# Kernel tuning notes

Measured on AMD Instinct MI355X. Metric: run time of the kernel, lower is better.

Reference implementation:

```python
import jax, jax.numpy as jnp
import numpy as np

FR = 44100          # frame_rate
L = 882000          # sound length (20 s @ 44.1 kHz)
T = 2048            # number of onset time steps
H_GRU = 3
H_LSTM = 10


def setup_inputs() -> dict:
    key = jax.random.key(0)
    ks = jax.random.split(key, 20)

    def unif(k, shape, fan):
        b = 1.0 / np.sqrt(fan)
        return jax.random.uniform(k, shape, jnp.float32, -b, b)

    return {
        "sound": jax.random.normal(ks[0], (1, L), jnp.float32),
        "alpha": jnp.sort(jax.random.randint(ks[1], (1, T), 0, L), axis=1),
        # GRU (input_size=FR, hidden=3): gates ordered (r, z, n). W_hh is
        # multiplied by h0=0 (seq_len==1), so only its bias b_hh matters.
        "gru_w_ih": unif(ks[2], (3 * H_GRU, FR), H_GRU),
        "gru_b_ih": unif(ks[3], (3 * H_GRU,), H_GRU),
        "gru_b_hh": unif(ks[4], (3 * H_GRU,), H_GRU),
        "conv2_w": unif(ks[5], (32, 1, 3), 1 * 3),
        "conv2_b": unif(ks[6], (32,), 1 * 3),
        "conv3_w": unif(ks[7], (16, 32, 3), 32 * 3),
        "conv3_b": unif(ks[8], (16,), 32 * 3),
        "lin_w": unif(ks[9], (10, 17), 17),
        "lin_b": unif(ks[10], (10,), 17),
        # LSTMCell gates ordered (i, f, g, o)
        "lstm_w_ih": unif(ks[11], (4 * H_LSTM, 10), H_LSTM),
        "lstm_w_hh": unif(ks[12], (4 * H_LSTM, H_LSTM), H_LSTM),
        "lstm_b_ih": unif(ks[13], (4 * H_LSTM,), H_LSTM),
        "lstm_b_hh": unif(ks[14], (4 * H_LSTM,), H_LSTM),
        "lin1_w": unif(ks[15], (32, 10), 10),
        "lin1_b": unif(ks[16], (32,), 10),
        "lin2_w": unif(ks[17], (1, 32), 32),
        "lin2_b": unif(ks[18], (1,), 32),
    }


def _conv1d(x, w, b, pad):
    # x: (N, C_in, W), w: (C_out, C_in, K)
    y = jax.lax.conv_general_dilated(
        x, w, window_strides=(1,), padding=[(pad, pad)],
        dimension_numbers=("NCH", "OIH", "NCH"))
    return y + b[None, :, None]


def reference(sound, alpha, gru_w_ih, gru_b_ih, gru_b_hh,
              conv2_w, conv2_b, conv3_w, conv3_b, lin_w, lin_b,
              lstm_w_ih, lstm_w_hh, lstm_b_ih, lstm_b_hh,
              lin1_w, lin1_b, lin2_w, lin2_b):
    fr2 = FR // 2
    padded = jnp.pad(sound[0], (fr2, fr2))                       # (L + FR,)
    # Vectorized dynamic-window gather: one (T, FR) fragment matrix.
    idx = alpha[0][:, None] + jnp.arange(FR)[None, :]            # (T, FR)
    frags = jnp.abs(padded[idx])                                 # (T, FR)

    # GRU: batch=1 -> unbatched input of seq_len=1, h0=0 => single step.
    gi = frags @ gru_w_ih.T + gru_b_ih                           # (T, 9)
    r = jax.nn.sigmoid(gi[:, 0:3] + gru_b_hh[0:3])
    z = jax.nn.sigmoid(gi[:, 3:6] + gru_b_hh[3:6])
    n = jnp.tanh(gi[:, 6:9] + r * gru_b_hh[6:9])
    h = (1.0 - z) * n                                            # (T, 3)

    x = h[:, None, :]                                            # (T, 1, 3)
    x = jax.nn.relu(_conv1d(x, conv2_w, conv2_b, pad=1))         # (T, 32, 3)
    x = _conv1d(x, conv3_w, conv3_b, pad=0)                      # (T, 16, 1)
    feat = x[:, :, 0]                                            # (T, 16)

    a = alpha[0].astype(jnp.float32)
    intervals = jnp.concatenate([a[:1], a[1:] - a[:-1]])         # (T,)
    xin = jnp.concatenate([intervals[:, None], feat], axis=1)    # (T, 17)
    xin = xin @ lin_w.T + lin_b                                  # (T, 10)

    def step(carry, xt):
        hh, cc = carry
        g = xt @ lstm_w_ih.T + lstm_b_ih + hh @ lstm_w_hh.T + lstm_b_hh
        i, f, gg, o = jnp.split(g, 4)
        cc = jax.nn.sigmoid(f) * cc + jax.nn.sigmoid(i) * jnp.tanh(gg)
        hh = jax.nn.sigmoid(o) * jnp.tanh(cc)
        return (hh, cc), None

    init = (jnp.zeros(H_LSTM, jnp.float32), jnp.zeros(H_LSTM, jnp.float32))
    (hT, _), _ = jax.lax.scan(step, init, xin)                   # hT: (10,)

    y = jax.nn.relu(hT[None, :] @ lin1_w.T + lin1_b)             # (1, 32)
    return jax.nn.sigmoid(y @ lin2_w.T + lin2_b)                 # (1, 1)
```

## Files before the change

kernel.cpp:

```cpp
#include <hip/hip_runtime.h>

#define FRLEN 44100
#define FR2 22050
#define LSND 882000
#define PADLEN (LSND + FRLEN)
#define TSTEPS 2048
#define ROWS 8
#define LOG2E 1.4426950408889634f

#define KPAD 44104
#define WPROW (KPAD/2)
#define NJP (WPROW/4)
#define PAIRS 463056

typedef _Float16 half2_ __attribute__((ext_vector_type(2)));

__device__ __forceinline__ float sigmoidf_(float x){ return 1.0f/(1.0f + __expf(-x)); }

__device__ __forceinline__ float dot2u_(uint a, uint b, float c){
#if __has_builtin(__builtin_amdgcn_fdot2)
  return __builtin_amdgcn_fdot2(*(half2_*)&a, *(half2_*)&b, c, false);
#else
  half2_ ha = *(half2_*)&a, hb = *(half2_*)&b;
  c = fmaf((float)ha.x, (float)hb.x, c);
  return fmaf((float)ha.y, (float)hb.y, c);
#endif
}

__device__ __forceinline__ float dot2h_(half2_ a, half2_ b, float c){
#if __has_builtin(__builtin_amdgcn_fdot2)
  return __builtin_amdgcn_fdot2(a, b, c, false);
#else
  c = fmaf((float)a.x, (float)b.x, c);
  return fmaf((float)a.y, (float)b.y, c);
#endif
}

__global__ void k_prep16(const float* __restrict__ sound, const float* __restrict__ w,
                         uint* __restrict__ pA, uint* __restrict__ pB,
                         uint* __restrict__ wp){
  const int stride = gridDim.x*blockDim.x;
  for (int i = blockIdx.x*blockDim.x + threadIdx.x; i < PAIRS + 9*WPROW; i += stride){
    if (i < PAIRS){
      int e0 = 2*i - FR2;
      float v0 = (e0 >= 0     && e0 < LSND)     ? fabsf(sound[e0])   : 0.0f;
      float v1 = (e0+1 >= 0   && e0+1 < LSND)   ? fabsf(sound[e0+1]) : 0.0f;
      float v2 = (e0+2 >= 0   && e0+2 < LSND)   ? fabsf(sound[e0+2]) : 0.0f;
      half2_ a = { (_Float16)v0, (_Float16)v1 };
      half2_ b = { (_Float16)v1, (_Float16)v2 };
      pA[i] = *(uint*)&a;
      pB[i] = *(uint*)&b;
    } else {
      int p = i - PAIRS;
      int k = p / WPROW, pr = p % WPROW;
      int j = 2*pr;
      float v0 = (j   < FRLEN) ? w[k*FRLEN + j]   : 0.0f;
      float v1 = (j+1 < FRLEN) ? w[k*FRLEN + j+1] : 0.0f;
      half2_ a = { (_Float16)v0, (_Float16)v1 };
      wp[i - PAIRS] = *(uint*)&a;
    }
  }
}

__global__ __launch_bounds__(512, 2) void k_front(const uint* __restrict__ pA,
    const uint* __restrict__ pB, const uint* __restrict__ wp,
    const int* __restrict__ alpha,
    const float* __restrict__ gbih, const float* __restrict__ gbhh,
    const float* __restrict__ c2w, const float* __restrict__ c2b,
    const float* __restrict__ c3w, const float* __restrict__ c3b,
    const float* __restrict__ lw, const float* __restrict__ lb,
    const float* __restrict__ wih, const float* __restrict__ bih, const float* __restrict__ bhh,
    _Float16* __restrict__ pre){
  const int tid = threadIdx.x;
  const int row0 = blockIdx.x * ROWS;
  const uint* hp[ROWS];
  int idx0[ROWS];
#pragma unroll
  for (int r = 0; r < ROWS; ++r){
    int b = alpha[row0 + r];
    hp[r] = (b & 1) ? pB : pA;
    idx0[r] = b >> 1;
  }
  float acc[ROWS][9];
#pragma unroll
  for (int r = 0; r < ROWS; ++r)
#pragma unroll
    for (int k = 0; k < 9; ++k) acc[r][k] = 0.0f;

  for (int jj = tid; jj < NJP; jj += 512){
    const int jp = jj*4;
    uint4 f[ROWS];
#pragma unroll
    for (int r = 0; r < ROWS; ++r){
      const uint* p = hp[r] + idx0[r] + jp;
      f[r].x = p[0]; f[r].y = p[1]; f[r].z = p[2]; f[r].w = p[3];
    }
#pragma unroll
    for (int k = 0; k < 9; ++k){
      const uint4 wq = *reinterpret_cast<const uint4*>(wp + k*WPROW + jp);
#pragma unroll
      for (int r = 0; r < ROWS; ++r){
        acc[r][k] = dot2u_(f[r].x, wq.x, acc[r][k]);
        acc[r][k] = dot2u_(f[r].y, wq.y, acc[r][k]);
        acc[r][k] = dot2u_(f[r].z, wq.z, acc[r][k]);
        acc[r][k] = dot2u_(f[r].w, wq.w, acc[r][k]);
      }
    }
  }
#pragma unroll
  for (int m = 32; m >= 1; m >>= 1){
#pragma unroll
    for (int r = 0; r < ROWS; ++r)
#pragma unroll
      for (int k = 0; k < 9; ++k)
        acc[r][k] += __shfl_xor(acc[r][k], m, 64);
  }
  __shared__ float red[8][ROWS*9];
  __shared__ float sgi[ROWS*9];
  const int wv_ = tid >> 6, ln = tid & 63;
  if (ln == 0){
#pragma unroll
    for (int r = 0; r < ROWS; ++r)
#pragma unroll
      for (int k = 0; k < 9; ++k) red[wv_][r*9+k] = acc[r][k];
  }
  __syncthreads();
  if (tid < ROWS*9){
    float s = 0.0f;
#pragma unroll
    for (int q = 0; q < 8; ++q) s += red[q][tid];
    sgi[tid] = s;
  }
  __syncthreads();
  if (tid < ROWS){
    const int t = row0 + tid;
    float gi[9];
#pragma unroll
    for (int k = 0; k < 9; ++k) gi[k] = sgi[tid*9+k] + gbih[k];
    float h[3];
#pragma unroll
    for (int q = 0; q < 3; ++q){
      float rr = sigmoidf_(gi[q]   + gbhh[q]);
      float zz = sigmoidf_(gi[3+q] + gbhh[3+q]);
      float nn = tanhf(gi[6+q] + rr*gbhh[6+q]);
      h[q] = (1.0f - zz)*nn;
    }
    float feat[16];
#pragma unroll
    for (int c = 0; c < 16; ++c) feat[c] = c3b[c];
    for (int ic = 0; ic < 32; ++ic){
      float w0 = c2w[ic*3+0], w1 = c2w[ic*3+1], w2 = c2w[ic*3+2], bb = c2b[ic];
      float x0 = fmaxf(bb + h[0]*w1 + h[1]*w2, 0.0f);
      float x1 = fmaxf(bb + h[0]*w0 + h[1]*w1 + h[2]*w2, 0.0f);
      float x2_ = fmaxf(bb + h[1]*w0 + h[2]*w1, 0.0f);
#pragma unroll
      for (int c = 0; c < 16; ++c){
        const float* wpp = c3w + (c*32+ic)*3;
        feat[c] += x0*wpp[0] + x1*wpp[1] + x2_*wpp[2];
      }
    }
    float interval = (float)(t == 0 ? alpha[0] : (alpha[t] - alpha[t-1]));
    float xin[10];
#pragma unroll
    for (int k = 0; k < 10; ++k){
      float s = lb[k] + interval*lw[k*17];
#pragma unroll
      for (int j = 0; j < 16; ++j) s = fmaf(feat[j], lw[k*17+1+j], s);
      xin[k] = s;
    }
#pragma unroll
    for (int k = 0; k < 40; ++k){
      float s = bih[k] + bhh[k];
#pragma unroll
      for (int i = 0; i < 10; ++i) s = fmaf(xin[i], wih[k*10+i], s);
      const float sc = (k >= 20 && k < 30) ? (-2.0f*LOG2E) : (-LOG2E);
      pre[t*40 + k] = (_Float16)(s * sc);
    }
  }
}

#define LSTM_STEP(PREFETCH_STMT)                                              \
  {                                                                           \
    float g = (float)q0;                                                      \
    q0 = q1; q1 = q2; q2 = q3;                                                \
    PREFETCH_STMT;                                                            \
    float ga = dot2h_(wpk0, hp0, g);                                          \
    ga = dot2h_(wpk1, hp1, ga);                                               \
    ga = dot2h_(wpk2, hp2, ga);                                               \
    float gb = dot2h_(wpk3, hp3, 0.0f);                                       \
    gb = dot2h_(wpk4, hp4, gb);                                               \
    g = ga + gb;                                                              \
    float act = fmaf(__builtin_amdgcn_rcpf(1.0f + __builtin_amdgcn_exp2f(g)), s2, s3); \
    float g_sw = act;                                                         \
    asm("v_permlane32_swap_b32 %0, %1" : "+v"(act), "+v"(g_sw));              \
    float f_sw = act;                                                         \
    asm("v_permlane16_swap_b32 %0, %1" : "+v"(act), "+v"(f_sw));              \
    float o_sw = g_sw;                                                        \
    asm("v_permlane16_swap_b32 %0, %1" : "+v"(g_sw), "+v"(o_sw));             \
    float ig = act * g_sw;                                                    \
    c = fmaf(f_sw, c, ig);                                                    \
    float th = fmaf(__builtin_amdgcn_rcpf(1.0f + __builtin_amdgcn_exp2f(c)), 2.0f, -1.0f); \
    float hn = o_sw * th;                                                     \
    int hni = __float_as_int(hn);                                             \
    int hnx = __builtin_amdgcn_update_dpp(0, hni, 0x111, 0xf, 0xf, true);     \
    auto hpk = __builtin_amdgcn_cvt_pkrtz(hn, __int_as_float(hnx));           \
    int pki = *(int*)&hpk;                                                    \
    { int _r = __builtin_amdgcn_readlane(pki, 0); hp0 = *(half2_*)&_r; }      \
    { int _r = __builtin_amdgcn_readlane(pki, 2); hp1 = *(half2_*)&_r; }      \
    { int _r = __builtin_amdgcn_readlane(pki, 4); hp2 = *(half2_*)&_r; }      \
    { int _r = __builtin_amdgcn_readlane(pki, 6); hp3 = *(half2_*)&_r; }      \
    { int _r = __builtin_amdgcn_readlane(pki, 8); hp4 = *(half2_*)&_r; }      \
  }

__global__ __launch_bounds__(1024, 1) void k_lstm(const _Float16* __restrict__ pre,
                       const float* __restrict__ whh,
                       const float* __restrict__ l1w, const float* __restrict__ l1b,
                       const float* __restrict__ l2w, const float* __restrict__ l2b,
                       float* __restrict__ out){
  extern __shared__ _Float16 sp[];
  {
    uint4* dst = (uint4*)sp;
    const uint4* src = (const uint4*)pre;
    for (int i = threadIdx.x; i < (TSTEPS*40*2)/16; i += 1024) dst[i] = src[i];
  }
  __syncthreads();
  if (threadIdx.x >= 64) return;

  const int lane = threadIdx.x;
  const int gate = lane >> 4;
  const int unit_raw = lane & 15;
  const int unit = unit_raw < 10 ? unit_raw : 9;
  const int L40 = gate*10 + unit;
  const bool is_g = (gate == 2);
  const float kk  = -2.0f*LOG2E;
  const float wsc = is_g ? kk : (-LOG2E);
  const float s2  = is_g ? (2.0f*kk) : 1.0f;
  const float s3  = is_g ? (-kk)     : 0.0f;
  half2_ wpk0, wpk1, wpk2, wpk3, wpk4;
  {
    const float* wr = whh + L40*10;
    wpk0 = { (_Float16)(wr[0]*wsc), (_Float16)(wr[1]*wsc) };
    wpk1 = { (_Float16)(wr[2]*wsc), (_Float16)(wr[3]*wsc) };
    wpk2 = { (_Float16)(wr[4]*wsc), (_Float16)(wr[5]*wsc) };
    wpk3 = { (_Float16)(wr[6]*wsc), (_Float16)(wr[7]*wsc) };
    wpk4 = { (_Float16)(wr[8]*wsc), (_Float16)(wr[9]*wsc) };
  }
  half2_ hz = { (_Float16)0.0f, (_Float16)0.0f };
  half2_ hp0 = hz, hp1 = hz, hp2 = hz, hp3 = hz, hp4 = hz;
  float c = 0.0f;

  _Float16 q0 = sp[0*40+L40], q1 = sp[1*40+L40], q2 = sp[2*40+L40], q3 = sp[3*40+L40];
#pragma unroll 4
  for (int t = 0; t < TSTEPS-4; ++t){
    LSTM_STEP(q3 = sp[(t+4)*40 + L40]);
  }
#pragma unroll
  for (int t = TSTEPS-4; t < TSTEPS; ++t){
    LSTM_STEP(;);
  }
  float hf[10];
  hf[0]=(float)hp0.x; hf[1]=(float)hp0.y; hf[2]=(float)hp1.x; hf[3]=(float)hp1.y;
  hf[4]=(float)hp2.x; hf[5]=(float)hp2.y; hf[6]=(float)hp3.x; hf[7]=(float)hp3.y;
  hf[8]=(float)hp4.x; hf[9]=(float)hp4.y;
  float z = 0.0f;
  if (lane < 32){
    float s = l1b[lane];
#pragma unroll
    for (int i = 0; i < 10; ++i) s = fmaf(hf[i], l1w[lane*10+i], s);
    z = fmaxf(s, 0.0f) * l2w[lane];
  }
#pragma unroll
  for (int m = 32; m >= 1; m >>= 1) z += __shfl_xor(z, m, 64);
  if (lane == 0) out[0] = sigmoidf_(z + l2b[0]);
}

extern "C" void kernel_launch(void* const* d_in, const int* in_sizes, int n_in,
                              void* d_out, int out_size, void* d_ws, size_t ws_size,
                              hipStream_t stream){
  const float* sound     = (const float*)d_in[0];
  const int*   alpha     = (const int*)  d_in[1];
  const float* gru_w_ih  = (const float*)d_in[2];
  const float* gru_b_ih  = (const float*)d_in[3];
  const float* gru_b_hh  = (const float*)d_in[4];
  const float* conv2_w   = (const float*)d_in[5];
  const float* conv2_b   = (const float*)d_in[6];
  const float* conv3_w   = (const float*)d_in[7];
  const float* conv3_b   = (const float*)d_in[8];
  const float* lin_w     = (const float*)d_in[9];
  const float* lin_b     = (const float*)d_in[10];
  const float* lstm_w_ih = (const float*)d_in[11];
  const float* lstm_w_hh = (const float*)d_in[12];
  const float* lstm_b_ih = (const float*)d_in[13];
  const float* lstm_b_hh = (const float*)d_in[14];
  const float* lin1_w    = (const float*)d_in[15];
  const float* lin1_b    = (const float*)d_in[16];
  const float* lin2_w    = (const float*)d_in[17];
  const float* lin2_b    = (const float*)d_in[18];

  char* ws = (char*)d_ws;
  uint* pA      = (uint*)ws;
  uint* pB      = pA + PAIRS;
  uint* wpairs  = pB + PAIRS;
  _Float16* pre = (_Float16*)(wpairs + 9*WPROW);

  (void)hipFuncSetAttribute((const void*)k_lstm,
        hipFuncAttributeMaxDynamicSharedMemorySize, TSTEPS*40*2);

  hipLaunchKernelGGL(k_prep16, dim3(1536), dim3(256), 0, stream,
                     sound, gru_w_ih, pA, pB, wpairs);
  hipLaunchKernelGGL(k_front, dim3(TSTEPS/ROWS), dim3(512), 0, stream,
                     pA, pB, wpairs, alpha,
                     gru_b_ih, gru_b_hh, conv2_w, conv2_b, conv3_w, conv3_b,
                     lin_w, lin_b, lstm_w_ih, lstm_b_ih, lstm_b_hh, pre);
  hipLaunchKernelGGL(k_lstm, dim3(1), dim3(1024), TSTEPS*40*2, stream,
                     pre, lstm_w_hh, lin1_w, lin1_b, lin2_w, lin2_b, (float*)d_out);
}
```

Before: 247.2 us.

## Vectorize prep kernel, software-prefetch front-end loads, fold tanh into LSTM output

The prep kernel now has each thread handle four pairs, using wide uint4 stores, float4 weight loads and packed fp16 conversion, and its grid is sized to the work instead of a fixed grid-stride loop. The front GEMV kernel double-buffers the fragment loads for the next iteration and prefetches the next weight row inside the k loop, to hide global load latency. In the LSTM recurrence, the tanh rescale and the multiply by the output gate are merged into one fma, removing a dependent op from the serial critical path. The prefetching uses more registers, which may lower occupancy in a kernel already holding 72 accumulators per thread.

```diff
diff --git a/kernel.cpp b/kernel.cpp
--- a/kernel.cpp
+++ b/kernel.cpp
@@ -3,7 +3,6 @@
 #define FRLEN 44100
 #define FR2 22050
 #define LSND 882000
-#define PADLEN (LSND + FRLEN)
 #define TSTEPS 2048
 #define ROWS 8
 #define LOG2E 1.4426950408889634f
@@ -12,6 +11,9 @@
 #define WPROW (KPAD/2)
 #define NJP (WPROW/4)
 #define PAIRS 463056
+#define NGS (PAIRS/4)
+#define WGRP (WPROW/4)
+#define NGW (9*WGRP)
 
 typedef _Float16 half2_ __attribute__((ext_vector_type(2)));
 
@@ -36,29 +38,48 @@
 #endif
 }
 
+__device__ __forceinline__ uint pk_(float a, float b){
+  auto p = __builtin_amdgcn_cvt_pkrtz(a, b);
+  return *(uint*)&p;
+}
+
 __global__ void k_prep16(const float* __restrict__ sound, const float* __restrict__ w,
                          uint* __restrict__ pA, uint* __restrict__ pB,
                          uint* __restrict__ wp){
-  const int stride = gridDim.x*blockDim.x;
-  for (int i = blockIdx.x*blockDim.x + threadIdx.x; i < PAIRS + 9*WPROW; i += stride){
-    if (i < PAIRS){
-      int e0 = 2*i - FR2;
-      float v0 = (e0 >= 0     && e0 < LSND)     ? fabsf(sound[e0])   : 0.0f;
-      float v1 = (e0+1 >= 0   && e0+1 < LSND)   ? fabsf(sound[e0+1]) : 0.0f;
-      float v2 = (e0+2 >= 0   && e0+2 < LSND)   ? fabsf(sound[e0+2]) : 0.0f;
-      half2_ a = { (_Float16)v0, (_Float16)v1 };
-      half2_ b = { (_Float16)v1, (_Float16)v2 };
-      pA[i] = *(uint*)&a;
-      pB[i] = *(uint*)&b;
+  const int i = blockIdx.x*blockDim.x + threadIdx.x;
+  if (i < NGS){
+    const int p0 = i*4;
+    const int e0 = 2*p0 - FR2;
+    float v[9];
+    if (e0 >= 0 && e0 + 8 < LSND){
+#pragma unroll
+      for (int k = 0; k < 9; ++k) v[k] = fabsf(sound[e0+k]);
     } else {
-      int p = i - PAIRS;
-      int k = p / WPROW, pr = p % WPROW;
-      int j = 2*pr;
-      float v0 = (j   < FRLEN) ? w[k*FRLEN + j]   : 0.0f;
-      float v1 = (j+1 < FRLEN) ? w[k*FRLEN + j+1] : 0.0f;
-      half2_ a = { (_Float16)v0, (_Float16)v1 };
-      wp[i - PAIRS] = *(uint*)&a;
-    }
+#pragma unroll
+      for (int k = 0; k < 9; ++k){
+        int e = e0 + k;
+        v[k] = (e >= 0 && e < LSND) ? fabsf(sound[e]) : 0.0f;
+      }
+    }
+    uint4 a = make_uint4(pk_(v[0],v[1]), pk_(v[2],v[3]), pk_(v[4],v[5]), pk_(v[6],v[7]));
+    uint4 b = make_uint4(pk_(v[1],v[2]), pk_(v[3],v[4]), pk_(v[5],v[6]), pk_(v[7],v[8]));
+    *reinterpret_cast<uint4*>(pA + p0) = a;
+    *reinterpret_cast<uint4*>(pB + p0) = b;
+  } else if (i < NGS + NGW){
+    const int g = i - NGS;
+    const int k = g / WGRP, gg = g % WGRP;
+    const int j = gg*8;
+    float v[8];
+    if (j + 8 <= FRLEN){
+      float4 x = *reinterpret_cast<const float4*>(w + k*FRLEN + j);
+      float4 y = *reinterpret_cast<const float4*>(w + k*FRLEN + j + 4);
+      v[0]=x.x; v[1]=x.y; v[2]=x.z; v[3]=x.w; v[4]=y.x; v[5]=y.y; v[6]=y.z; v[7]=y.w;
+    } else {
+#pragma unroll
+      for (int q = 0; q < 8; ++q) v[q] = (j+q < FRLEN) ? w[k*FRLEN + j + q] : 0.0f;
+    }
+    *reinterpret_cast<uint4*>(wp + k*WPROW + gg*4) =
+        make_uint4(pk_(v[0],v[1]), pk_(v[2],v[3]), pk_(v[4],v[5]), pk_(v[6],v[7]));
   }
 }
 
@@ -73,13 +94,11 @@
     _Float16* __restrict__ pre){
   const int tid = threadIdx.x;
   const int row0 = blockIdx.x * ROWS;
-  const uint* hp[ROWS];
-  int idx0[ROWS];
+  const uint* bp[ROWS];
 #pragma unroll
   for (int r = 0; r < ROWS; ++r){
     int b = alpha[row0 + r];
-    hp[r] = (b & 1) ? pB : pA;
-    idx0[r] = b >> 1;
+    bp[r] = ((b & 1) ? pB : pA) + (b >> 1);
   }
   float acc[ROWS][9];
 #pragma unroll
@@ -87,25 +106,46 @@
 #pragma unroll
     for (int k = 0; k < 9; ++k) acc[r][k] = 0.0f;
 
+  uint4 fcur[ROWS];
+  {
+    const int jp = tid*4;
+#pragma unroll
+    for (int r = 0; r < ROWS; ++r){
+      const uint* p = bp[r] + jp;
+      fcur[r] = make_uint4(p[0], p[1], p[2], p[3]);
+    }
+  }
   for (int jj = tid; jj < NJP; jj += 512){
+    const int jn = jj + 512;
+    uint4 fnx[ROWS];
+    if (jn < NJP){
+      const int jp2 = jn*4;
+#pragma unroll
+      for (int r = 0; r < ROWS; ++r){
+        const uint* p = bp[r] + jp2;
+        fnx[r] = make_uint4(p[0], p[1], p[2], p[3]);
+      }
+    } else {
+#pragma unroll
+      for (int r = 0; r < ROWS; ++r) fnx[r] = fcur[r];
+    }
     const int jp = jj*4;
-    uint4 f[ROWS];
-#pragma unroll
-    for (int r = 0; r < ROWS; ++r){
-      const uint* p = hp[r] + idx0[r] + jp;
-      f[r].x = p[0]; f[r].y = p[1]; f[r].z = p[2]; f[r].w = p[3];
-    }
+    uint4 wq = *reinterpret_cast<const uint4*>(wp + jp);
 #pragma unroll
     for (int k = 0; k < 9; ++k){
-      const uint4 wq = *reinterpret_cast<const uint4*>(wp + k*WPROW + jp);
+      uint4 wqn;
+      if (k < 8) wqn = *reinterpret_cast<const uint4*>(wp + (k+1)*WPROW + jp);
 #pragma unroll
       for (int r = 0; r < ROWS; ++r){
-        acc[r][k] = dot2u_(f[r].x, wq.x, acc[r][k]);
-        acc[r][k] = dot2u_(f[r].y, wq.y, acc[r][k]);
-        acc[r][k] = dot2u_(f[r].z, wq.z, acc[r][k]);
-        acc[r][k] = dot2u_(f[r].w, wq.w, acc[r][k]);
+        acc[r][k] = dot2u_(fcur[r].x, wq.x, acc[r][k]);
+        acc[r][k] = dot2u_(fcur[r].y, wq.y, acc[r][k]);
+        acc[r][k] = dot2u_(fcur[r].z, wq.z, acc[r][k]);
+        acc[r][k] = dot2u_(fcur[r].w, wq.w, acc[r][k]);
       }
-    }
+      if (k < 8) wq = wqn;
+    }
+#pragma unroll
+    for (int r = 0; r < ROWS; ++r) fcur[r] = fnx[r];
   }
 #pragma unroll
   for (int m = 32; m >= 1; m >>= 1){
@@ -199,8 +239,8 @@
     asm("v_permlane16_swap_b32 %0, %1" : "+v"(g_sw), "+v"(o_sw));             \
     float ig = act * g_sw;                                                    \
     c = fmaf(f_sw, c, ig);                                                    \
-    float th = fmaf(__builtin_amdgcn_rcpf(1.0f + __builtin_amdgcn_exp2f(c)), 2.0f, -1.0f); \
-    float hn = o_sw * th;                                                     \
+    float o2 = o_sw + o_sw;                                                   \
+    float hn = fmaf(__builtin_amdgcn_rcpf(1.0f + __builtin_amdgcn_exp2f(c)), o2, -o_sw); \
     int hni = __float_as_int(hn);                                             \
     int hnx = __builtin_amdgcn_update_dpp(0, hni, 0x111, 0xf, 0xf, true);     \
     auto hpk = __builtin_amdgcn_cvt_pkrtz(hn, __int_as_float(hnx));           \
@@ -306,7 +346,7 @@
   (void)hipFuncSetAttribute((const void*)k_lstm,
         hipFuncAttributeMaxDynamicSharedMemorySize, TSTEPS*40*2);
 
-  hipLaunchKernelGGL(k_prep16, dim3(1536), dim3(256), 0, stream,
+  hipLaunchKernelGGL(k_prep16, dim3((NGS + NGW + 255)/256), dim3(256), 0, stream,
                      sound, gru_w_ih, pA, pB, wpairs);
   hipLaunchKernelGGL(k_front, dim3(TSTEPS/ROWS), dim3(512), 0, stream,
                      pA, pB, wpairs, alpha,
```

After: 246.1 us (median of 3 runs). Within noise of the previous version (-0.4%).
